# Kernel tuning notes

Hardware: AMD Instinct MI355X
Metric: run time of the kernel (lower is better)

Reference implementation:

```python
import jax, jax.numpy as jnp
import numpy as np

B, N, E = 64, 256, 512   # batch, leaves (power of 2), embed_size
D, U = 512, 512          # tree_size, units (controller size == units)


def setup_inputs() -> dict:
    key = jax.random.key(0)
    ks = jax.random.split(key, 11)
    sc = lambda k, shape: jax.random.normal(k, shape, dtype=jnp.float32) * 0.05
    return {
        "inputs": jax.random.normal(ks[0], (B, N, E), dtype=jnp.float32),
        "h0": sc(ks[1], (B, U)),
        "c0": sc(ks[2], (B, U)),
        "W_t": sc(ks[3], (E, D)),          # Transformer
        "W_j": sc(ks[4], (2 * D, D)),      # Join
        "W_s": sc(ks[5], (D + U, 1)),      # Search
        "W_h": sc(ks[6], (D + U, D)),      # Write candidate
        "W_T": sc(ks[7], (D + U, 1)),      # Write gate
        "kernel": sc(ks[8], (E, 4 * U)),   # LSTM input kernel (i,f,c,o)
        "rec_kernel": sc(ks[9], (U, 4 * U)),
        "bias": jnp.zeros((4 * U,), jnp.float32),
    }


def reference(inputs, h0, c0, W_t, W_j, W_s, W_h, W_T, kernel, rec_kernel, bias):
    b, n, e = inputs.shape
    control = h0  # control = previous LSTM hidden state

    # --- leaf embed: Transformer, batched over all leaves ---
    leaf_h = jax.nn.relu(jnp.einsum('bne,ed->bnd', inputs, W_t))  # [B,N,D]

    # --- refresh: bottom-up join, batched per tree level ---
    levels = [leaf_h]
    h = leaf_h
    while h.shape[1] > 1:
        pair = jnp.concatenate([h[:, 0::2], h[:, 1::2]], axis=-1)  # [B,m/2,2D]
        h = jax.nn.relu(jnp.einsum('bmk,kd->bmd', pair, W_j))
        levels.append(h)

    # --- retrieve: top-down search producing leaf attentions ---
    # Searches all use refresh-time h (parent search happens before any
    # update in its subtree), so a level-batched top-down pass is exact.
    attn = jnp.ones((b, 1, 1), inputs.dtype)
    for lvl in range(len(levels) - 1, 0, -1):
        node_h = levels[lvl]                     # [B,m,D]
        m = node_h.shape[1]
        ctrl = jnp.broadcast_to(control[:, None, :], (b, m, control.shape[-1]))
        mr = jax.nn.sigmoid(jnp.einsum('bmk,ko->bmo',
                                       jnp.concatenate([node_h, ctrl], -1), W_s))  # [B,m,1]
        # children interleave: left gets attn*(1-mr), right gets attn*mr
        attn = jnp.concatenate([attn * (1.0 - mr), attn * mr], axis=-1).reshape(b, 2 * m, 1)

    tree_out = jnp.sum(attn * inputs, axis=1)  # [B,E] soft-retrieved leaf value

    # --- write update of leaf memories, batched over all leaves ---
    ctrl = jnp.broadcast_to(control[:, None, :], (b, n, control.shape[-1]))
    data = jnp.concatenate([leaf_h, ctrl], -1)                     # [B,N,D+U]
    cand = jax.nn.sigmoid(jnp.einsum('bnk,kd->bnd', data, W_h))
    upd = jax.nn.sigmoid(jnp.einsum('bnk,ko->bno', data, W_T))
    written = upd * cand + (1.0 - upd) * leaf_h
    leaf_h_new = attn * written + (1.0 - attn) * leaf_h            # [B,N,D]

    # --- LSTM cell update (keras LSTMCell gate order i,f,c,o) ---
    z = tree_out @ kernel + h0 @ rec_kernel + bias
    zi, zf, zg, zo = jnp.split(z, 4, axis=-1)
    c_new = jax.nn.sigmoid(zf) * c0 + jax.nn.sigmoid(zi) * jnp.tanh(zg)
    h_new = jax.nn.sigmoid(zo) * jnp.tanh(c_new)
    return h_new, c_new, leaf_h_new
```

## Files before the change

### kernel.cpp

```cpp
#include <hip/hip_runtime.h>
#include <hip/hip_bf16.h>
#include <cstdint>
#include <cstddef>


__device__ __forceinline__ float sigmoidf_(float x) { return 1.0f / (1.0f + __expf(-x)); }

typedef __attribute__((ext_vector_type(8))) short bf16x8;
typedef __attribute__((ext_vector_type(4))) float f32x4;

__device__ __forceinline__ void load_lds16(const void* g, void* l) {
  __builtin_amdgcn_global_load_lds((const __attribute__((address_space(1))) void*)g,
                                   (__attribute__((address_space(3))) void*)l, 16, 0, 0);
}

__global__ __launch_bounds__(256)
void tconv_all(const float* __restrict__ W_t, const float* __restrict__ W_j,
               const float* __restrict__ W_h,
               __hip_bfloat16* __restrict__ Wt_t, __hip_bfloat16* __restrict__ Wt_j,
               __hip_bfloat16* __restrict__ Wt_h) {
  const int z = blockIdx.z;
  if (z != 1 && blockIdx.x >= 16) return;
  const int K = (z == 1) ? 1024 : 512;
  const float* W = (z == 0) ? W_t : ((z == 1) ? W_j : W_h);
  __hip_bfloat16* Wt = (z == 0) ? Wt_t : ((z == 1) ? Wt_j : Wt_h);
  __shared__ float sh[32][33];
  const int tx = threadIdx.x & 31, ty = threadIdx.x >> 5;
  const int k0 = blockIdx.x * 32, n0 = blockIdx.y * 32;
#pragma unroll
  for (int i = 0; i < 4; ++i)
    sh[ty + i * 8][tx] = W[(size_t)(k0 + ty + i * 8) * 512 + n0 + tx];
  __syncthreads();
#pragma unroll
  for (int i = 0; i < 4; ++i)
    Wt[(size_t)(n0 + ty + i * 8) * K + k0 + tx] = __float2bfloat16(sh[tx][ty + i * 8]);
}

template<int MODE, bool AFP32>
__global__ __launch_bounds__(256)
void mfma_gemm(const __hip_bfloat16* __restrict__ A, const float* __restrict__ Af,
               const __hip_bfloat16* __restrict__ Bt, int M, int K,
               __hip_bfloat16* __restrict__ Cb, float* __restrict__ Cf,
               const float* __restrict__ ctrl_h, const float* __restrict__ attn,
               const float* __restrict__ upd, const __hip_bfloat16* __restrict__ leaf) {
  __shared__ __align__(16) __hip_bfloat16 Asm[128 * 32];
  __shared__ __align__(16) __hip_bfloat16 Bsm[128 * 32];
  const int tid = threadIdx.x;
  const int wave = tid >> 6, lane = tid & 63;
  const int bm = blockIdx.y * 128, bn = blockIdx.x * 128;
  const int wm = (wave >> 1) * 64, wn = (wave & 1) * 64;
  const int q = lane >> 4, lr = lane & 15;

  f32x4 acc[4][4] = {};

  const int c0 = wave * 128 + lane, c1 = c0 + 64;
  const size_t ga0 = (size_t)(bm + (c0 >> 2)) * K + (c0 & 3) * 8;
  const size_t ga1 = (size_t)(bm + (c1 >> 2)) * K + (c1 & 3) * 8;
  const size_t gb0 = (size_t)(bn + (c0 >> 2)) * K + (c0 & 3) * 8;
  const size_t gb1 = (size_t)(bn + (c1 >> 2)) * K + (c1 & 3) * 8;
  __hip_bfloat16* la0 = Asm + wave * 1024;
  __hip_bfloat16* la1 = Asm + wave * 1024 + 512;
  __hip_bfloat16* lb0 = Bsm + wave * 1024;
  __hip_bfloat16* lb1 = Bsm + wave * 1024 + 512;

  for (int k0v = 0; k0v < K; k0v += 32) {
    if (AFP32) {
#pragma unroll
      for (int it = 0; it < 4; ++it) {
        const int c = it * 256 + tid;
        const int row = c >> 3, kc = c & 7;
        float4 v = *(const float4*)(Af + (size_t)(bm + row) * K + k0v + kc * 4);
        __hip_bfloat16 h[4] = {__float2bfloat16(v.x), __float2bfloat16(v.y),
                               __float2bfloat16(v.z), __float2bfloat16(v.w)};
        *(ushort4*)(Asm + row * 32 + kc * 4) = *(ushort4*)h;
      }
    } else {
      load_lds16(A + ga0 + k0v, la0);
      load_lds16(A + ga1 + k0v, la1);
    }
    load_lds16(Bt + gb0 + k0v, lb0);
    load_lds16(Bt + gb1 + k0v, lb1);
    __syncthreads();
    bf16x8 af[4], bfr[4];
#pragma unroll
    for (int mt = 0; mt < 4; ++mt)
      af[mt] = *(const bf16x8*)(Asm + (wm + mt * 16 + lr) * 32 + q * 8);
#pragma unroll
    for (int nt = 0; nt < 4; ++nt)
      bfr[nt] = *(const bf16x8*)(Bsm + (wn + nt * 16 + lr) * 32 + q * 8);
#pragma unroll
    for (int mt = 0; mt < 4; ++mt)
#pragma unroll
      for (int nt = 0; nt < 4; ++nt)
        acc[mt][nt] = __builtin_amdgcn_mfma_f32_16x16x32_bf16(af[mt], bfr[nt], acc[mt][nt], 0, 0, 0);
    __syncthreads();
  }

  if (MODE == 0) {
#pragma unroll
    for (int mt = 0; mt < 4; ++mt) {
      const int rbase = bm + wm + mt * 16 + q * 4;
#pragma unroll
      for (int nt = 0; nt < 4; ++nt) {
        const int col = bn + wn + nt * 16 + lr;
#pragma unroll
        for (int r = 0; r < 4; ++r) {
          const int row = rbase + r;
          if (row < M)
            Cb[(size_t)row * 512 + col] = __float2bfloat16(fmaxf(acc[mt][nt][r], 0.f));
        }
      }
    }
  } else {
#pragma unroll
    for (int mt = 0; mt < 4; ++mt) {
      const int rbase = bm + wm + mt * 16 + q * 4;
#pragma unroll
      for (int r = 0; r < 4; ++r) {
        const int row = rbase + r;
        const float a = attn[row];
        const float u = upd[row];
        const int bidx = row >> 8;
#pragma unroll
        for (int nt = 0; nt < 4; ++nt) {
          const int col = bn + wn + nt * 16 + lr;
          const float cand = sigmoidf_(acc[mt][nt][r] + ctrl_h[(size_t)bidx * 512 + col]);
          const float lf = __bfloat162float(leaf[(size_t)row * 512 + col]);
          const float w = u * cand + (1.f - u) * lf;
          Cf[(size_t)row * 512 + col] = a * w + (1.f - a) * lf;
        }
      }
    }
  }
}

__global__ __launch_bounds__(256)
void join_level(const __hip_bfloat16* __restrict__ in, __hip_bfloat16* __restrict__ outp,
                const __hip_bfloat16* __restrict__ Wt_j) {
  const int wave = threadIdx.x >> 6, lane = threadIdx.x & 63;
  const int q = lane >> 4, lr = lane & 15;
  const int tile = blockIdx.x * 4 + wave;
  const int mtile = tile >> 5, ntile = tile & 31;
  const __hip_bfloat16* ap = in + (size_t)(mtile * 16 + lr) * 1024 + q * 8;
  const __hip_bfloat16* bp = Wt_j + (size_t)(ntile * 16 + lr) * 1024 + q * 8;
  f32x4 acc = {0.f, 0.f, 0.f, 0.f};
#pragma unroll 8
  for (int k0 = 0; k0 < 1024; k0 += 32) {
    bf16x8 a  = *(const bf16x8*)(ap + k0);
    bf16x8 bb = *(const bf16x8*)(bp + k0);
    acc = __builtin_amdgcn_mfma_f32_16x16x32_bf16(a, bb, acc, 0, 0, 0);
  }
  const int col = ntile * 16 + lr;
  const int orow = mtile * 16 + q * 4;
#pragma unroll
  for (int r = 0; r < 4; ++r)
    outp[(size_t)(orow + r) * 512 + col] = __float2bfloat16(fmaxf(acc[r], 0.f));
}

__global__ __launch_bounds__(256)
void gemv_dual(const __hip_bfloat16* __restrict__ leaf,
               const __hip_bfloat16* __restrict__ levels,
               const float* __restrict__ W_T, const float* __restrict__ W_s,
               const float* __restrict__ ctrlT,
               float* __restrict__ upd, float* __restrict__ sc) {
  const int wave = threadIdx.x >> 6, lane = threadIdx.x & 63;
  const int bid = blockIdx.x;
  const bool is_upd = bid < 4096;
  const int row = (is_upd ? bid : (bid - 4096)) * 4 + wave;
  const __hip_bfloat16* X = is_upd ? leaf : levels;
  const float* w = is_upd ? W_T : W_s;
  union { bf16x8 v; __hip_bfloat16 e[8]; } u;
  u.v = *(const bf16x8*)(X + (size_t)row * 512 + lane * 8);
  const float* wp = w + lane * 8;
  float p = 0.f;
#pragma unroll
  for (int j = 0; j < 8; ++j) p += __bfloat162float(u.e[j]) * wp[j];
#pragma unroll
  for (int off = 32; off > 0; off >>= 1) p += __shfl_down(p, off);
  if (lane == 0) {
    if (is_upd) upd[row] = sigmoidf_(p + ctrlT[row >> 8]);
    else        sc[row] = p;
  }
}

__global__ __launch_bounds__(256)
void prep_ctrl(const float* __restrict__ h0, const float* __restrict__ W_T,
               float* __restrict__ ctrlT) {
  const int b = blockIdx.x, tid = threadIdx.x;
  __shared__ float part[256];
  float p = 0.f;
  for (int i = tid; i < 512; i += 256) p += h0[b * 512 + i] * W_T[512 + i];
  part[tid] = p; __syncthreads();
  for (int s = 128; s > 0; s >>= 1) { if (tid < s) part[tid] += part[tid + s]; __syncthreads(); }
  if (tid == 0) ctrlT[b] = part[0];
}

__global__ __launch_bounds__(256)
void propagate(const float* __restrict__ sc, const float* __restrict__ h0,
               const float* __restrict__ W_s, float* __restrict__ attn_out) {
  const int b = blockIdx.x, tid = threadIdx.x;
  __shared__ float part[256], attn_sh[256], newattn[256];
  __shared__ float scs;
  float p = 0.f;
  for (int i = tid; i < 512; i += 256) p += h0[b * 512 + i] * W_s[512 + i];
  part[tid] = p; __syncthreads();
  for (int s = 128; s > 0; s >>= 1) { if (tid < s) part[tid] += part[tid + s]; __syncthreads(); }
  if (tid == 0) { scs = part[0]; attn_sh[0] = 1.f; }
  __syncthreads();
  const int row_off[9] = {0, 0, 8192, 12288, 14336, 15360, 15872, 16128, 16256};
#pragma unroll
  for (int l = 8; l >= 1; --l) {
    const int m = 256 >> l;
    if (tid < m) {
      const float mr = sigmoidf_(sc[row_off[l] + b * m + tid] + scs);
      const float a = attn_sh[tid];
      newattn[2 * tid]     = a * (1.f - mr);
      newattn[2 * tid + 1] = a * mr;
    }
    __syncthreads();
    if (tid < 2 * m) attn_sh[tid] = newattn[tid];
    __syncthreads();
  }
  attn_out[b * 256 + tid] = attn_sh[tid];
}

__global__ __launch_bounds__(256)
void tree_part(const float* __restrict__ inputs, const float* __restrict__ attn,
               float* __restrict__ tp) {
  const int s = blockIdx.x, b = blockIdx.y;
  const int tid = threadIdx.x;
  __shared__ float a_sh[64];
  if (tid < 64) a_sh[tid] = attn[b * 256 + s * 64 + tid];
  __syncthreads();
  float acc0 = 0.f, acc1 = 0.f;
  const float* base = inputs + ((size_t)b * 256 + s * 64) * 512;
  for (int nn = 0; nn < 64; ++nn) {
    const float a = a_sh[nn];
    const float* row = base + (size_t)nn * 512;
    acc0 += a * row[tid];
    acc1 += a * row[tid + 256];
  }
  tp[((size_t)s * 64 + b) * 512 + tid]       = acc0;
  tp[((size_t)s * 64 + b) * 512 + tid + 256] = acc1;
}

__global__ __launch_bounds__(256)
void tree_reduce(const float* __restrict__ tp, float* __restrict__ tre) {
  const int i = blockIdx.x * 256 + threadIdx.x;
  tre[i] = tp[i] + tp[32768 + i] + tp[65536 + i] + tp[98304 + i];
}

__global__ __launch_bounds__(256)
void ctrl_gemm(const float* __restrict__ h0, const float* __restrict__ W_h,
               float* __restrict__ chp) {
  const int col = blockIdx.x * 256 + threadIdx.x;
  const int b   = blockIdx.y;
  const int z   = blockIdx.z;
  __shared__ float hsh[128];
  if (threadIdx.x < 128) hsh[threadIdx.x] = h0[b * 512 + z * 128 + threadIdx.x];
  __syncthreads();
  const float* Wp = W_h + (size_t)(512 + z * 128) * 512 + col;
  float s = 0.f;
#pragma unroll 8
  for (int k = 0; k < 128; ++k) s += hsh[k] * Wp[(size_t)k * 512];
  chp[((size_t)z * 64 + b) * 512 + col] = s;
}

__global__ __launch_bounds__(256)
void ctrl_reduce(const float* __restrict__ chp, float* __restrict__ ch) {
  const int i = blockIdx.x * 256 + threadIdx.x;
  ch[i] = chp[i] + chp[32768 + i] + chp[65536 + i] + chp[98304 + i];
}

__global__ __launch_bounds__(256)
void lstm_gemm_splitk(const float* __restrict__ tre, const float* __restrict__ h0,
                      const float* __restrict__ kern, const float* __restrict__ rec,
                      float* __restrict__ Zp) {
  const int tid = threadIdx.x;
  const int col = blockIdx.x * 256 + tid;
  const int b0 = blockIdx.y * 4;
  const int z = blockIdx.z;
  const float* X = (z < 4) ? tre : h0;
  const float* W = (z < 4) ? (kern + (size_t)z * 128 * 2048)
                           : (rec + (size_t)(z - 4) * 128 * 2048);
  const int koff = (z & 3) * 128;
  __shared__ float xs[4][128];
  for (int i = tid; i < 512; i += 256) {
    int bb = i >> 7, k = i & 127;
    xs[bb][k] = X[(b0 + bb) * 512 + koff + k];
  }
  __syncthreads();
  float a0 = 0.f, a1 = 0.f, a2 = 0.f, a3 = 0.f;
#pragma unroll 8
  for (int k = 0; k < 128; ++k) {
    const float w = W[(size_t)k * 2048 + col];
    a0 += xs[0][k] * w;
    a1 += xs[1][k] * w;
    a2 += xs[2][k] * w;
    a3 += xs[3][k] * w;
  }
  Zp[((size_t)z * 64 + b0 + 0) * 2048 + col] = a0;
  Zp[((size_t)z * 64 + b0 + 1) * 2048 + col] = a1;
  Zp[((size_t)z * 64 + b0 + 2) * 2048 + col] = a2;
  Zp[((size_t)z * 64 + b0 + 3) * 2048 + col] = a3;
}

__global__ __launch_bounds__(256)
void lstm_combine(const float* __restrict__ Zp, const float* __restrict__ bias,
                  const float* __restrict__ c0,
                  float* __restrict__ out_h, float* __restrict__ out_c) {
  const int i = blockIdx.x * 256 + threadIdx.x;
  const int b = i >> 9, u = i & 511;
  float zi = bias[u], zf = bias[512 + u], zg = bias[1024 + u], zo = bias[1536 + u];
#pragma unroll
  for (int z = 0; z < 8; ++z) {
    const size_t base = ((size_t)z * 64 + b) * 2048;
    zi += Zp[base + u];
    zf += Zp[base + 512 + u];
    zg += Zp[base + 1024 + u];
    zo += Zp[base + 1536 + u];
  }
  const float c = sigmoidf_(zf) * c0[i] + sigmoidf_(zi) * tanhf(zg);
  out_h[i] = sigmoidf_(zo) * tanhf(c);
  out_c[i] = c;
}

extern "C" void kernel_launch(void* const* d_in, const int* in_sizes, int n_in,
                              void* d_out, int out_size, void* d_ws, size_t ws_size,
                              hipStream_t stream) {
  const float* inputs = (const float*)d_in[0];
  const float* h0     = (const float*)d_in[1];
  const float* c0     = (const float*)d_in[2];
  const float* W_t    = (const float*)d_in[3];
  const float* W_j    = (const float*)d_in[4];
  const float* W_s    = (const float*)d_in[5];
  const float* W_h    = (const float*)d_in[6];
  const float* W_T    = (const float*)d_in[7];
  const float* kern   = (const float*)d_in[8];
  const float* rec    = (const float*)d_in[9];
  const float* bias   = (const float*)d_in[10];
  float* out = (float*)d_out;

  char* p = (char*)d_ws;
  __hip_bfloat16* leaf_bf   = (__hip_bfloat16*)p; p += 16777216;
  __hip_bfloat16* levels_bf = (__hip_bfloat16*)p; p += 16842752;
  __hip_bfloat16* Wt_t      = (__hip_bfloat16*)p; p += 524288;
  __hip_bfloat16* Wt_j      = (__hip_bfloat16*)p; p += 1048576;
  __hip_bfloat16* Wt_h      = (__hip_bfloat16*)p; p += 524288;
  float* attn  = (float*)p; p += 65536;
  float* upd   = (float*)p; p += 65536;
  float* tre   = (float*)p; p += 131072;
  float* chp   = (float*)p; p += 524288;
  float* ch    = (float*)p; p += 131072;
  float* Zp    = (float*)p; p += 4194304;
  float* sc    = (float*)p; p += 65536;
  float* ctrlT = (float*)p; p += 4096;
  float* tp    = (float*)p; p += 524288;

  tconv_all<<<dim3(32, 16, 3), 256, 0, stream>>>(W_t, W_j, W_h, Wt_t, Wt_j, Wt_h);
  ctrl_gemm<<<dim3(2, 64, 4), 256, 0, stream>>>(h0, W_h, chp);
  ctrl_reduce<<<128, 256, 0, stream>>>(chp, ch);
  prep_ctrl<<<64, 256, 0, stream>>>(h0, W_T, ctrlT);

  mfma_gemm<0, true><<<dim3(4, 128), 256, 0, stream>>>(
      nullptr, inputs, Wt_t, 16384, 512,
      leaf_bf, nullptr, nullptr, nullptr, nullptr, nullptr);

  const int lvl_off_h[9] = {0, 0, 4194304, 6291456, 7340032,
                            7864320, 8126464, 8257536, 8323072};
  const __hip_bfloat16* Aptr = leaf_bf;
  for (int l = 1; l <= 3; ++l) {
    const int M = 64 * (256 >> l);
    __hip_bfloat16* Cl = levels_bf + lvl_off_h[l];
    mfma_gemm<0, false><<<dim3(4, M / 128), 256, 0, stream>>>(
        Aptr, nullptr, Wt_j, M, 1024,
        Cl, nullptr, nullptr, nullptr, nullptr, nullptr);
    Aptr = Cl;
  }
  for (int l = 4; l <= 8; ++l) {
    const int m_out = 256 >> l;
    join_level<<<32 * m_out, 256, 0, stream>>>(levels_bf + lvl_off_h[l - 1],
                                               levels_bf + lvl_off_h[l], Wt_j);
  }

  gemv_dual<<<8176, 256, 0, stream>>>(leaf_bf, levels_bf, W_T, W_s, ctrlT, upd, sc);
  propagate<<<64, 256, 0, stream>>>(sc, h0, W_s, attn);

  tree_part<<<dim3(4, 64), 256, 0, stream>>>(inputs, attn, tp);
  tree_reduce<<<128, 256, 0, stream>>>(tp, tre);

  mfma_gemm<1, false><<<dim3(4, 128), 256, 0, stream>>>(
      leaf_bf, nullptr, Wt_h, 16384, 512,
      nullptr, out + 65536, ch, attn, upd, leaf_bf);
  lstm_gemm_splitk<<<dim3(8, 16, 8), 256, 0, stream>>>(tre, h0, kern, rec, Zp);
  lstm_combine<<<128, 256, 0, stream>>>(Zp, bias, c0, out, out + 32768);
}
```

Before: 332.5 us.

## Fuse tree tail join levels and small reduction kernels to cut launches

Replaces the five per-level join launches for levels 4-8 with one kernel per batch that keeps intermediate levels in LDS and chains them. The ctrl reduction and ctrlT prep move into ctrl_gemm and the write GEMM epilogue, and tree_part/tree_reduce merge into propagate. This removes several kernel launches and small global round trips. In exchange, the fused join runs on only 64 blocks and rereads Wt_j from global at every level, and tree_out now uses one block per batch walking 256 rows serially, which lowers parallelism.

```diff
diff --git a/kernel.cpp b/kernel.cpp
--- a/kernel.cpp
+++ b/kernel.cpp
@@ -9,7 +9,7 @@
 typedef __attribute__((ext_vector_type(8))) short bf16x8;
 typedef __attribute__((ext_vector_type(4))) float f32x4;
 
-__device__ __forceinline__ void load_lds16(const void* g, void* l) {
+__device__ __forceinline__ void load_lds16b(const void* g, void* l) {
   __builtin_amdgcn_global_load_lds((const __attribute__((address_space(1))) void*)g,
                                    (__attribute__((address_space(3))) void*)l, 16, 0, 0);
 }
@@ -41,15 +41,25 @@
 void mfma_gemm(const __hip_bfloat16* __restrict__ A, const float* __restrict__ Af,
                const __hip_bfloat16* __restrict__ Bt, int M, int K,
                __hip_bfloat16* __restrict__ Cb, float* __restrict__ Cf,
-               const float* __restrict__ ctrl_h, const float* __restrict__ attn,
-               const float* __restrict__ upd, const __hip_bfloat16* __restrict__ leaf) {
+               const float* __restrict__ chp, const float* __restrict__ ctrlT,
+               const float* __restrict__ attn, const float* __restrict__ upd_raw,
+               const __hip_bfloat16* __restrict__ leaf) {
   __shared__ __align__(16) __hip_bfloat16 Asm[128 * 32];
   __shared__ __align__(16) __hip_bfloat16 Bsm[128 * 32];
+  __shared__ float ch_sh[128];
   const int tid = threadIdx.x;
   const int wave = tid >> 6, lane = tid & 63;
   const int bm = blockIdx.y * 128, bn = blockIdx.x * 128;
   const int wm = (wave >> 1) * 64, wn = (wave & 1) * 64;
   const int q = lane >> 4, lr = lane & 15;
+  const int bidx = bm >> 8;
+
+  if (MODE == 1 && tid < 128) {
+    ch_sh[tid] = chp[(size_t)(0 * 64 + bidx) * 512 + bn + tid]
+               + chp[(size_t)(1 * 64 + bidx) * 512 + bn + tid]
+               + chp[(size_t)(2 * 64 + bidx) * 512 + bn + tid]
+               + chp[(size_t)(3 * 64 + bidx) * 512 + bn + tid];
+  }
 
   f32x4 acc[4][4] = {};
 
@@ -75,11 +85,11 @@
         *(ushort4*)(Asm + row * 32 + kc * 4) = *(ushort4*)h;
       }
     } else {
-      load_lds16(A + ga0 + k0v, la0);
-      load_lds16(A + ga1 + k0v, la1);
-    }
-    load_lds16(Bt + gb0 + k0v, lb0);
-    load_lds16(Bt + gb1 + k0v, lb1);
+      load_lds16b(A + ga0 + k0v, la0);
+      load_lds16b(A + ga1 + k0v, la1);
+    }
+    load_lds16b(Bt + gb0 + k0v, lb0);
+    load_lds16b(Bt + gb1 + k0v, lb1);
     __syncthreads();
     bf16x8 af[4], bfr[4];
 #pragma unroll
@@ -112,6 +122,7 @@
       }
     }
   } else {
+    const float cT = ctrlT[bidx];
 #pragma unroll
     for (int mt = 0; mt < 4; ++mt) {
       const int rbase = bm + wm + mt * 16 + q * 4;
@@ -119,12 +130,11 @@
       for (int r = 0; r < 4; ++r) {
         const int row = rbase + r;
         const float a = attn[row];
-        const float u = upd[row];
-        const int bidx = row >> 8;
+        const float u = sigmoidf_(upd_raw[row] + cT);
 #pragma unroll
         for (int nt = 0; nt < 4; ++nt) {
           const int col = bn + wn + nt * 16 + lr;
-          const float cand = sigmoidf_(acc[mt][nt][r] + ctrl_h[(size_t)bidx * 512 + col]);
+          const float cand = sigmoidf_(acc[mt][nt][r] + ch_sh[wn + nt * 16 + lr]);
           const float lf = __bfloat162float(leaf[(size_t)row * 512 + col]);
           const float w = u * cand + (1.f - u) * lf;
           Cf[(size_t)row * 512 + col] = a * w + (1.f - a) * lf;
@@ -135,34 +145,67 @@
 }
 
 __global__ __launch_bounds__(256)
-void join_level(const __hip_bfloat16* __restrict__ in, __hip_bfloat16* __restrict__ outp,
-                const __hip_bfloat16* __restrict__ Wt_j) {
-  const int wave = threadIdx.x >> 6, lane = threadIdx.x & 63;
+void join_tail45678(const __hip_bfloat16* __restrict__ lvl3,
+                    __hip_bfloat16* __restrict__ levels,
+                    const __hip_bfloat16* __restrict__ Wt_j) {
+  constexpr int STR = 520;
+  __shared__ __align__(16) __hip_bfloat16 bufA[32 * STR];
+  __shared__ __align__(16) __hip_bfloat16 bufB[16 * STR];
+  const int b = blockIdx.x;
+  const int tid = threadIdx.x;
+  const int wave = tid >> 6, lane = tid & 63;
   const int q = lane >> 4, lr = lane & 15;
-  const int tile = blockIdx.x * 4 + wave;
-  const int mtile = tile >> 5, ntile = tile & 31;
-  const __hip_bfloat16* ap = in + (size_t)(mtile * 16 + lr) * 1024 + q * 8;
-  const __hip_bfloat16* bp = Wt_j + (size_t)(ntile * 16 + lr) * 1024 + q * 8;
-  f32x4 acc = {0.f, 0.f, 0.f, 0.f};
-#pragma unroll 8
-  for (int k0 = 0; k0 < 1024; k0 += 32) {
-    bf16x8 a  = *(const bf16x8*)(ap + k0);
-    bf16x8 bb = *(const bf16x8*)(bp + k0);
-    acc = __builtin_amdgcn_mfma_f32_16x16x32_bf16(a, bb, acc, 0, 0, 0);
-  }
-  const int col = ntile * 16 + lr;
-  const int orow = mtile * 16 + q * 4;
-#pragma unroll
-  for (int r = 0; r < 4; ++r)
-    outp[(size_t)(orow + r) * 512 + col] = __float2bfloat16(fmaxf(acc[r], 0.f));
+
+  {
+    const __hip_bfloat16* src = lvl3 + (size_t)b * 32 * 512;
+    for (int i = tid; i < 32 * 64; i += 256) {
+      const int r = i >> 6, c = i & 63;
+      *(bf16x8*)(bufA + r * STR + c * 8) = *(const bf16x8*)(src + (size_t)r * 512 + c * 8);
+    }
+  }
+  __syncthreads();
+
+  const size_t off_e[9] = {0, 0, 4194304, 6291456, 7340032,
+                           7864320, 8126464, 8257536, 8323072};
+  __hip_bfloat16* cur = bufA;
+  __hip_bfloat16* nxt = bufB;
+  int m_out = 16;
+  for (int l = 4; l <= 8; ++l, m_out >>= 1) {
+    const int arow = (lr < m_out) ? lr : 0;
+    f32x4 acc[8] = {};
+    for (int k0 = 0; k0 < 1024; k0 += 32) {
+      const int kk = k0 + q * 8;
+      const bf16x8 a = *(const bf16x8*)(cur + (2 * arow + (kk >> 9)) * STR + (kk & 511));
+#pragma unroll
+      for (int j = 0; j < 8; ++j) {
+        const bf16x8 bb = *(const bf16x8*)(Wt_j + (size_t)((wave * 8 + j) * 16 + lr) * 1024 + kk);
+        acc[j] = __builtin_amdgcn_mfma_f32_16x16x32_bf16(a, bb, acc[j], 0, 0, 0);
+      }
+    }
+    __hip_bfloat16* gout = levels + off_e[l] + (size_t)b * m_out * 512;
+#pragma unroll
+    for (int j = 0; j < 8; ++j) {
+      const int col = (wave * 8 + j) * 16 + lr;
+#pragma unroll
+      for (int r = 0; r < 4; ++r) {
+        const int row = q * 4 + r;
+        if (row < m_out) {
+          const __hip_bfloat16 v = __float2bfloat16(fmaxf(acc[j][r], 0.f));
+          nxt[row * STR + col] = v;
+          gout[(size_t)row * 512 + col] = v;
+        }
+      }
+    }
+    __syncthreads();
+    __hip_bfloat16* t = cur; cur = nxt; nxt = t;
+  }
 }
 
 __global__ __launch_bounds__(256)
 void gemv_dual(const __hip_bfloat16* __restrict__ leaf,
                const __hip_bfloat16* __restrict__ levels,
                const float* __restrict__ W_T, const float* __restrict__ W_s,
-               const float* __restrict__ ctrlT,
-               float* __restrict__ upd, float* __restrict__ sc) {
+               float* __restrict__ upd_raw, float* __restrict__ sc) {
   const int wave = threadIdx.x >> 6, lane = threadIdx.x & 63;
   const int bid = blockIdx.x;
   const bool is_upd = bid < 4096;
@@ -178,26 +221,42 @@
 #pragma unroll
   for (int off = 32; off > 0; off >>= 1) p += __shfl_down(p, off);
   if (lane == 0) {
-    if (is_upd) upd[row] = sigmoidf_(p + ctrlT[row >> 8]);
+    if (is_upd) upd_raw[row] = p;
     else        sc[row] = p;
   }
 }
 
 __global__ __launch_bounds__(256)
-void prep_ctrl(const float* __restrict__ h0, const float* __restrict__ W_T,
-               float* __restrict__ ctrlT) {
-  const int b = blockIdx.x, tid = threadIdx.x;
+void ctrl_gemm(const float* __restrict__ h0, const float* __restrict__ W_h,
+               const float* __restrict__ W_T,
+               float* __restrict__ chp, float* __restrict__ ctrlT) {
+  const int col = blockIdx.x * 256 + threadIdx.x;
+  const int b   = blockIdx.y;
+  const int z   = blockIdx.z;
+  __shared__ float hsh[128];
   __shared__ float part[256];
-  float p = 0.f;
-  for (int i = tid; i < 512; i += 256) p += h0[b * 512 + i] * W_T[512 + i];
-  part[tid] = p; __syncthreads();
-  for (int s = 128; s > 0; s >>= 1) { if (tid < s) part[tid] += part[tid + s]; __syncthreads(); }
-  if (tid == 0) ctrlT[b] = part[0];
-}
-
-__global__ __launch_bounds__(256)
-void propagate(const float* __restrict__ sc, const float* __restrict__ h0,
-               const float* __restrict__ W_s, float* __restrict__ attn_out) {
+  if (threadIdx.x < 128) hsh[threadIdx.x] = h0[b * 512 + z * 128 + threadIdx.x];
+  __syncthreads();
+  const float* Wp = W_h + (size_t)(512 + z * 128) * 512 + col;
+  float s = 0.f;
+#pragma unroll 8
+  for (int k = 0; k < 128; ++k) s += hsh[k] * Wp[(size_t)k * 512];
+  chp[((size_t)z * 64 + b) * 512 + col] = s;
+
+  if (z == 0 && blockIdx.x == 0) {
+    const int tid = threadIdx.x;
+    float p2 = 0.f;
+    for (int i = tid; i < 512; i += 256) p2 += h0[b * 512 + i] * W_T[512 + i];
+    part[tid] = p2; __syncthreads();
+    for (int st = 128; st > 0; st >>= 1) { if (tid < st) part[tid] += part[tid + st]; __syncthreads(); }
+    if (tid == 0) ctrlT[b] = part[0];
+  }
+}
+
+__global__ __launch_bounds__(256)
+void propagate_tree(const float* __restrict__ sc, const float* __restrict__ h0,
+                    const float* __restrict__ W_s, const float* __restrict__ inputs,
+                    float* __restrict__ attn_out, float* __restrict__ tre) {
   const int b = blockIdx.x, tid = threadIdx.x;
   __shared__ float part[256], attn_sh[256], newattn[256];
   __shared__ float scs;
@@ -222,54 +281,17 @@
     __syncthreads();
   }
   attn_out[b * 256 + tid] = attn_sh[tid];
-}
-
-__global__ __launch_bounds__(256)
-void tree_part(const float* __restrict__ inputs, const float* __restrict__ attn,
-               float* __restrict__ tp) {
-  const int s = blockIdx.x, b = blockIdx.y;
-  const int tid = threadIdx.x;
-  __shared__ float a_sh[64];
-  if (tid < 64) a_sh[tid] = attn[b * 256 + s * 64 + tid];
-  __syncthreads();
+
   float acc0 = 0.f, acc1 = 0.f;
-  const float* base = inputs + ((size_t)b * 256 + s * 64) * 512;
-  for (int nn = 0; nn < 64; ++nn) {
-    const float a = a_sh[nn];
-    const float* row = base + (size_t)nn * 512;
-    acc0 += a * row[tid];
-    acc1 += a * row[tid + 256];
-  }
-  tp[((size_t)s * 64 + b) * 512 + tid]       = acc0;
-  tp[((size_t)s * 64 + b) * 512 + tid + 256] = acc1;
-}
-
-__global__ __launch_bounds__(256)
-void tree_reduce(const float* __restrict__ tp, float* __restrict__ tre) {
-  const int i = blockIdx.x * 256 + threadIdx.x;
-  tre[i] = tp[i] + tp[32768 + i] + tp[65536 + i] + tp[98304 + i];
-}
-
-__global__ __launch_bounds__(256)
-void ctrl_gemm(const float* __restrict__ h0, const float* __restrict__ W_h,
-               float* __restrict__ chp) {
-  const int col = blockIdx.x * 256 + threadIdx.x;
-  const int b   = blockIdx.y;
-  const int z   = blockIdx.z;
-  __shared__ float hsh[128];
-  if (threadIdx.x < 128) hsh[threadIdx.x] = h0[b * 512 + z * 128 + threadIdx.x];
-  __syncthreads();
-  const float* Wp = W_h + (size_t)(512 + z * 128) * 512 + col;
-  float s = 0.f;
-#pragma unroll 8
-  for (int k = 0; k < 128; ++k) s += hsh[k] * Wp[(size_t)k * 512];
-  chp[((size_t)z * 64 + b) * 512 + col] = s;
-}
-
-__global__ __launch_bounds__(256)
-void ctrl_reduce(const float* __restrict__ chp, float* __restrict__ ch) {
-  const int i = blockIdx.x * 256 + threadIdx.x;
-  ch[i] = chp[i] + chp[32768 + i] + chp[65536 + i] + chp[98304 + i];
+  const float* base = inputs + (size_t)b * 256 * 512;
+#pragma unroll 4
+  for (int n = 0; n < 256; ++n) {
+    const float a = attn_sh[n];
+    acc0 += a * base[(size_t)n * 512 + tid];
+    acc1 += a * base[(size_t)n * 512 + tid + 256];
+  }
+  tre[b * 512 + tid]       = acc0;
+  tre[b * 512 + tid + 256] = acc1;
 }
 
 __global__ __launch_bounds__(256)
@@ -348,50 +370,41 @@
   __hip_bfloat16* Wt_j      = (__hip_bfloat16*)p; p += 1048576;
   __hip_bfloat16* Wt_h      = (__hip_bfloat16*)p; p += 524288;
   float* attn  = (float*)p; p += 65536;
-  float* upd   = (float*)p; p += 65536;
+  float* updr  = (float*)p; p += 65536;
   float* tre   = (float*)p; p += 131072;
   float* chp   = (float*)p; p += 524288;
-  float* ch    = (float*)p; p += 131072;
   float* Zp    = (float*)p; p += 4194304;
   float* sc    = (float*)p; p += 65536;
   float* ctrlT = (float*)p; p += 4096;
-  float* tp    = (float*)p; p += 524288;
-
-  tconv_all<<<dim3(32, 16, 3), 256, 0, stream>>>(W_t, W_j, W_h, Wt_t, Wt_j, Wt_h);
-  ctrl_gemm<<<dim3(2, 64, 4), 256, 0, stream>>>(h0, W_h, chp);
-  ctrl_reduce<<<128, 256, 0, stream>>>(chp, ch);
-  prep_ctrl<<<64, 256, 0, stream>>>(h0, W_T, ctrlT);
-
-  mfma_gemm<0, true><<<dim3(4, 128), 256, 0, stream>>>(
-      nullptr, inputs, Wt_t, 16384, 512,
-      leaf_bf, nullptr, nullptr, nullptr, nullptr, nullptr);
 
   const int lvl_off_h[9] = {0, 0, 4194304, 6291456, 7340032,
                             7864320, 8126464, 8257536, 8323072};
+
+  tconv_all<<<dim3(32, 16, 3), 256, 0, stream>>>(W_t, W_j, W_h, Wt_t, Wt_j, Wt_h);
+  ctrl_gemm<<<dim3(2, 64, 4), 256, 0, stream>>>(h0, W_h, W_T, chp, ctrlT);
+
+  mfma_gemm<0, true><<<dim3(4, 128), 256, 0, stream>>>(
+      nullptr, inputs, Wt_t, 16384, 512, leaf_bf, nullptr,
+      nullptr, nullptr, nullptr, nullptr, nullptr);
+
   const __hip_bfloat16* Aptr = leaf_bf;
   for (int l = 1; l <= 3; ++l) {
     const int M = 64 * (256 >> l);
     __hip_bfloat16* Cl = levels_bf + lvl_off_h[l];
     mfma_gemm<0, false><<<dim3(4, M / 128), 256, 0, stream>>>(
-        Aptr, nullptr, Wt_j, M, 1024,
-        Cl, nullptr, nullptr, nullptr, nullptr, nullptr);
+        Aptr, nullptr, Wt_j, M, 1024, Cl, nullptr,
+        nullptr, nullptr, nullptr, nullptr, nullptr);
     Aptr = Cl;
   }
-  for (int l = 4; l <= 8; ++l) {
-    const int m_out = 256 >> l;
-    join_level<<<32 * m_out, 256, 0, stream>>>(levels_bf + lvl_off_h[l - 1],
-                                               levels_bf + lvl_off_h[l], Wt_j);
-  }
-
-  gemv_dual<<<8176, 256, 0, stream>>>(leaf_bf, levels_bf, W_T, W_s, ctrlT, upd, sc);
-  propagate<<<64, 256, 0, stream>>>(sc, h0, W_s, attn);
-
-  tree_part<<<dim3(4, 64), 256, 0, stream>>>(inputs, attn, tp);
-  tree_reduce<<<128, 256, 0, stream>>>(tp, tre);
+  join_tail45678<<<64, 256, 0, stream>>>(levels_bf + lvl_off_h[3], levels_bf, Wt_j);
+
+  gemv_dual<<<8176, 256, 0, stream>>>(leaf_bf, levels_bf, W_T, W_s, updr, sc);
+  propagate_tree<<<64, 256, 0, stream>>>(sc, h0, W_s, inputs, attn, tre);
 
   mfma_gemm<1, false><<<dim3(4, 128), 256, 0, stream>>>(
-      leaf_bf, nullptr, Wt_h, 16384, 512,
-      nullptr, out + 65536, ch, attn, upd, leaf_bf);
+      leaf_bf, nullptr, Wt_h, 16384, 512, nullptr, out + 65536,
+      chp, ctrlT, attn, updr, leaf_bf);
+
   lstm_gemm_splitk<<<dim3(8, 16, 8), 256, 0, stream>>>(tre, h0, kern, rec, Zp);
   lstm_combine<<<128, 256, 0, stream>>>(Zp, bias, c0, out, out + 32768);
 }
```

Measured after the change: 428.3 us. +28.8%, slower.
